# Optimization experiments

Hardware: AMD Instinct MI355X
Metric: run time of the kernel (lower is better)

The kernel has to match this reference:

```python
import jax, jax.numpy as jnp
import numpy as np

D_MODEL = 2048
NUM_HEADS = 16
D_K = D_MODEL // NUM_HEADS
THETA = 10000.0
MAX_SEQ_LEN = 2048
B, S = 2, 2048


def setup_inputs() -> dict:
    key = jax.random.key(0)
    ks = jax.random.split(key, 5)
    x = jax.random.normal(ks[0], (B, S, D_MODEL), dtype=jnp.float32)
    token_positions = jnp.tile(jnp.arange(S, dtype=jnp.int64 if jax.config.jax_enable_x64 else jnp.int32), (B, 1))
    wq = jax.random.normal(ks[1], (D_MODEL, D_MODEL), dtype=jnp.float32)
    wk = jax.random.normal(ks[2], (D_MODEL, D_MODEL), dtype=jnp.float32)
    wv = jax.random.normal(ks[3], (D_MODEL, D_MODEL), dtype=jnp.float32)
    wo = jax.random.normal(ks[4], (D_MODEL, D_MODEL), dtype=jnp.float32)
    return {"x": x, "token_positions": token_positions, "wq": wq, "wk": wk, "wv": wv, "wo": wo}


def _rope_tables():
    # inv freqs: exp(arange(0,d_k,2) * (-log(theta)/d_k))  -> [d_k/2]
    inv_freq = jnp.exp(jnp.arange(0, D_K, 2, dtype=jnp.float32) * (-np.log(THETA) / D_K))
    m = jnp.arange(MAX_SEQ_LEN, dtype=jnp.float32)[:, None]  # [L,1]
    ang = m * inv_freq[None, :]                               # [L, d_k/2]
    return jnp.cos(ang), jnp.sin(ang)


def _apply_rope(x, token_positions, cos_tab, sin_tab):
    # x: [B, H, S, d_k]; token_positions: [B, S]
    cos = cos_tab[token_positions][:, None, :, :]  # [B,1,S,d_k/2]
    sin = sin_tab[token_positions][:, None, :, :]
    xe = x[..., 0::2]
    xo = x[..., 1::2]
    re = xe * cos - xo * sin
    ro = xo * cos + xe * sin
    out = jnp.stack([re, ro], axis=-1).reshape(x.shape)
    return out


def reference(x, token_positions, wq, wk, wv, wo):
    b, s, _ = x.shape
    cos_tab, sin_tab = _rope_tables()

    def split_heads(t):  # [B,S,D] -> [B,H,S,d_k]
        return t.reshape(b, s, NUM_HEADS, D_K).transpose(0, 2, 1, 3)

    q = _apply_rope(split_heads(x @ wq), token_positions, cos_tab, sin_tab)
    k = _apply_rope(split_heads(x @ wk), token_positions, cos_tab, sin_tab)
    v = split_heads(x @ wv)

    scores = jnp.einsum("bhqd,bhkd->bhqk", q, k) / jnp.sqrt(jnp.float32(D_K))
    causal = jnp.tril(jnp.ones((s, s), dtype=bool))
    scores = jnp.where(causal[None, None], scores, jnp.float32(-1e9))
    attn = jax.nn.softmax(scores, axis=-1)
    out = jnp.einsum("bhqk,bhkd->bhqd", attn, v)
    out = out.transpose(0, 2, 1, 3).reshape(b, s, D_MODEL)
    return out @ wo
```

## Files before the change

kernel.cpp:

```cpp
#include <hip/hip_runtime.h>
#include <hip/hip_bf16.h>
#include <cstdio>

namespace {

constexpr int kSeq = 2048;
constexpr int kDModel = 2048;
constexpr int kHeads = 16;
constexpr int kDk = 128;
constexpr int kBatch = 2;
constexpr int kM = kBatch * kSeq;
constexpr float kQScale = 0.08838834764831845f;

typedef __bf16 bf16_t;
typedef __bf16 bf16x8 __attribute__((ext_vector_type(8)));
typedef __bf16 bf16x4 __attribute__((ext_vector_type(4)));
typedef float f32x4 __attribute__((ext_vector_type(4)));
typedef short s16x4 __attribute__((ext_vector_type(4)));

__device__ __forceinline__ f32x4 mfma32(bf16x8 a, bf16x8 b, f32x4 c) {
  return __builtin_amdgcn_mfma_f32_16x16x32_bf16(a, b, c, 0, 0, 0);
}

#if __has_builtin(__builtin_amdgcn_mfma_f32_16x16x16_bf16)
__device__ __forceinline__ f32x4 mfma16(bf16x4 a, bf16x4 b, f32x4 c) {
  return __builtin_amdgcn_mfma_f32_16x16x16_bf16(a, b, c, 0, 0, 0);
}
#else
__device__ __forceinline__ f32x4 mfma16(bf16x4 a, bf16x4 b, f32x4 c) {
  union U { bf16x4 b; s16x4 s; } ua, ub;
  ua.b = a; ub.b = b;
  return __builtin_amdgcn_mfma_f32_16x16x16bf16_1k(ua.s, ub.s, c, 0, 0, 0);
}
#endif

using gas_void = const __attribute__((address_space(1))) void;
using las_void = __attribute__((address_space(3))) void;

__device__ __forceinline__ void gload_lds16(const bf16_t* g, bf16_t* l) {
  __builtin_amdgcn_global_load_lds((gas_void*)g, (las_void*)l, 16, 0, 0);
}

__global__ void k_rope_table(float* __restrict__ cost, float* __restrict__ sint) {
  const int p = blockIdx.x;
  const int i = threadIdx.x;
  const double inv = exp(-(double)(2 * i) * 9.210340371976184 / 128.0);
  const double ang = (double)p * inv;
  cost[p * 64 + i] = (float)cos(ang);
  sint[p * 64 + i] = (float)sin(ang);
}

__global__ void k_split_x(const float* __restrict__ x, bf16_t* __restrict__ xh,
                          bf16_t* __restrict__ xl, int n) {
  const int idx = (blockIdx.x * blockDim.x + threadIdx.x) * 4;
  if (idx >= n) return;
  const float4 v = *(const float4*)(x + idx);
  const float vv[4] = {v.x, v.y, v.z, v.w};
  bf16x4 hv, lv;
#pragma unroll
  for (int j = 0; j < 4; ++j) {
    const bf16_t h = (bf16_t)vv[j];
    hv[j] = h;
    lv[j] = (bf16_t)(vv[j] - (float)h);
  }
  *(bf16x4*)(xh + idx) = hv;
  *(bf16x4*)(xl + idx) = lv;
}

__global__ void k_transpose_w(const float* __restrict__ w, bf16_t* __restrict__ wth,
                              bf16_t* __restrict__ wtl) {
  __shared__ float tile[32][33];
  const int bx = blockIdx.x * 32;
  const int by = blockIdx.y * 32;
  const int tx = threadIdx.x, ty = threadIdx.y;
#pragma unroll
  for (int i = 0; i < 32; i += 8)
    tile[ty + i][tx] = w[(size_t)(by + ty + i) * kDModel + bx + tx];
  __syncthreads();
#pragma unroll
  for (int i = 0; i < 32; i += 8) {
    const float v = tile[tx][ty + i];
    const size_t o = (size_t)(bx + ty + i) * kDModel + by + tx;
    const bf16_t h = (bf16_t)v;
    wth[o] = h;
    if (wtl) wtl[o] = (bf16_t)(v - (float)h);
  }
}

template <int TERMS, int EPI>
__global__ __launch_bounds__(256) void k_gemm(
    const bf16_t* __restrict__ Ah, const bf16_t* __restrict__ Al,
    const bf16_t* __restrict__ Bh, const bf16_t* __restrict__ Bl,
    void* __restrict__ O0, void* __restrict__ O1,
    const int* __restrict__ tokpos, const float* __restrict__ cost,
    const float* __restrict__ sint, float scale, int M, int N, int K) {
  __shared__ __align__(16) bf16_t sAh[128 * 32];
  __shared__ __align__(16) bf16_t sBh[128 * 32];
  __shared__ __align__(16) bf16_t sAl[TERMS == 3 ? 128 * 32 : 8];
  __shared__ __align__(16) bf16_t sBl[TERMS == 3 ? 128 * 32 : 8];

  const int tid = threadIdx.x;
  const int wid = tid >> 6;
  const int lane = tid & 63;
  const int lo = lane & 15, hi = lane >> 4;
  const int wr = wid >> 1, wc = wid & 1;
  const int flat = blockIdx.x + blockIdx.y * gridDim.x;
  const int wgid = (flat & 7) * ((gridDim.x * gridDim.y) >> 3) + (flat >> 3);
  const int m0 = (wgid / gridDim.x) * 128, n0 = (wgid % gridDim.x) * 128;

  f32x4 acc[4][4];
  const f32x4 z = {0.f, 0.f, 0.f, 0.f};
#pragma unroll
  for (int i = 0; i < 4; ++i)
#pragma unroll
    for (int j = 0; j < 4; ++j) acc[i][j] = z;

  const int rr = wid * 16 + (lane >> 2);
  const int kk = (lane & 3) * 8;

  for (int k0 = 0; k0 < K; k0 += 32) {
    __syncthreads();
    {
      const bf16_t* gA = Ah + (size_t)(m0 + rr) * K + k0 + kk;
      gload_lds16(gA, sAh + wid * 512);
      gload_lds16(gA + (size_t)64 * K, sAh + 2048 + wid * 512);
      const bf16_t* gB = Bh + (size_t)(n0 + rr) * K + k0 + kk;
      gload_lds16(gB, sBh + wid * 512);
      gload_lds16(gB + (size_t)64 * K, sBh + 2048 + wid * 512);
      if constexpr (TERMS == 3) {
        const bf16_t* gAl = Al + (size_t)(m0 + rr) * K + k0 + kk;
        gload_lds16(gAl, sAl + wid * 512);
        gload_lds16(gAl + (size_t)64 * K, sAl + 2048 + wid * 512);
        const bf16_t* gBl = Bl + (size_t)(n0 + rr) * K + k0 + kk;
        gload_lds16(gBl, sBl + wid * 512);
        gload_lds16(gBl + (size_t)64 * K, sBl + 2048 + wid * 512);
      }
    }
    __syncthreads();
    bf16x8 fah[4], fbh[4];
#pragma unroll
    for (int mi = 0; mi < 4; ++mi)
      fah[mi] = *(const bf16x8*)(sAh + (wr * 64 + mi * 16 + lo) * 32 + 8 * hi);
#pragma unroll
    for (int ni = 0; ni < 4; ++ni)
      fbh[ni] = *(const bf16x8*)(sBh + (wc * 64 + ni * 16 + lo) * 32 + 8 * hi);
    if constexpr (TERMS == 3) {
      bf16x8 fal[4], fbl[4];
#pragma unroll
      for (int mi = 0; mi < 4; ++mi)
        fal[mi] = *(const bf16x8*)(sAl + (wr * 64 + mi * 16 + lo) * 32 + 8 * hi);
#pragma unroll
      for (int ni = 0; ni < 4; ++ni)
        fbl[ni] = *(const bf16x8*)(sBl + (wc * 64 + ni * 16 + lo) * 32 + 8 * hi);
#pragma unroll
      for (int mi = 0; mi < 4; ++mi)
#pragma unroll
        for (int ni = 0; ni < 4; ++ni) {
          acc[mi][ni] = mfma32(fah[mi], fbh[ni], acc[mi][ni]);
          acc[mi][ni] = mfma32(fah[mi], fbl[ni], acc[mi][ni]);
          acc[mi][ni] = mfma32(fal[mi], fbh[ni], acc[mi][ni]);
        }
    } else {
#pragma unroll
      for (int mi = 0; mi < 4; ++mi)
#pragma unroll
        for (int ni = 0; ni < 4; ++ni)
          acc[mi][ni] = mfma32(fah[mi], fbh[ni], acc[mi][ni]);
    }
  }

  if constexpr (EPI == 0) {
    float* C = (float*)O0;
#pragma unroll
    for (int mi = 0; mi < 4; ++mi)
#pragma unroll
      for (int ni = 0; ni < 4; ++ni)
#pragma unroll
        for (int r = 0; r < 4; ++r) {
          const int row = m0 + wr * 64 + mi * 16 + hi * 4 + r;
          const int col = n0 + wc * 64 + ni * 16 + lo;
          C[(size_t)row * N + col] = acc[mi][ni][r];
        }
  } else if constexpr (EPI == 1) {
    bf16_t* Xh = (bf16_t*)O0;
    bf16_t* Xl = (bf16_t*)O1;
    const int is64 = (tokpos[1] == 0) ? 1 : 0;
#pragma unroll
    for (int mi = 0; mi < 4; ++mi) {
#pragma unroll
      for (int r = 0; r < 4; ++r) {
        const int row = m0 + wr * 64 + mi * 16 + hi * 4 + r;
        const int pos = is64 ? tokpos[2 * row] : tokpos[row];
#pragma unroll
        for (int ni = 0; ni < 4; ++ni) {
          const int col = n0 + wc * 64 + ni * 16 + lo;
          const float v = acc[mi][ni][r] * scale;
          const float pv = __shfl_xor(v, 1);
          const int ip = (col & 127) >> 1;
          const float c = cost[pos * 64 + ip];
          const float sn = sint[pos * 64 + ip];
          const float sgn = (lo & 1) ? sn : -sn;
          const float rv = v * c + pv * sgn;
          const bf16_t hb = (bf16_t)rv;
          const size_t o = (size_t)row * N + col;
          Xh[o] = hb;
          Xl[o] = (bf16_t)(rv - (float)hb);
        }
      }
    }
  } else {
    bf16_t* VT = (bf16_t*)O0;
#pragma unroll
    for (int mi = 0; mi < 4; ++mi)
#pragma unroll
      for (int ni = 0; ni < 4; ++ni) {
        const int col = n0 + wc * 64 + ni * 16 + lo;
        const int h = col >> 7, d = col & 127;
        const int rowb = m0 + wr * 64 + mi * 16 + hi * 4;
        const int b = rowb >> 11, s = rowb & (kSeq - 1);
        bf16x4 ov;
#pragma unroll
        for (int r = 0; r < 4; ++r) ov[r] = (bf16_t)acc[mi][ni][r];
        *(bf16x4*)(VT + ((size_t)((b * kHeads + h) * kDk + d)) * kSeq + s) = ov;
      }
  }
}

__global__ __launch_bounds__(256) void k_attn3(
    const bf16_t* __restrict__ Qh, const bf16_t* __restrict__ Ql,
    const bf16_t* __restrict__ Kh, const bf16_t* __restrict__ Kl,
    const bf16_t* __restrict__ VT, bf16_t* __restrict__ Ob) {
  __shared__ __align__(16) bf16_t sK[2][2][32 * 128];
  __shared__ __align__(16) bf16_t sV[2][128 * 32];

  const int tid = threadIdx.x;
  const int wid = tid >> 6, lane = tid & 63;
  const int lo = lane & 15, hi = lane >> 4;
  const int flat = blockIdx.x + blockIdx.y * gridDim.x;
  const int j = flat >> 3;
  const int bh = (flat & 7) * 4 + (j & 3);
  const int qi = 15 - (j >> 2);
  const int b = bh >> 4, h = bh & 15;
  const int q0 = qi * 128;
  const int qw = q0 + wid * 32;

  bf16x8 qhf[4][2], qlf[4][2];
  {
    const size_t qbase =
        (size_t)(b * kSeq + qw + lo) * kDModel + h * kDk + hi * 8;
#pragma unroll
    for (int qt = 0; qt < 2; ++qt)
#pragma unroll
      for (int ks = 0; ks < 4; ++ks) {
        const size_t o = qbase + (size_t)qt * 16 * kDModel + ks * 32;
        qhf[ks][qt] = *(const bf16x8*)(Qh + o);
        qlf[ks][qt] = *(const bf16x8*)(Ql + o);
      }
  }

  const int rK = wid * 8 + (lane >> 4);
  const int gK0 = ((lane & 15) ^ (rK & 7)) * 8;
  const bf16_t* pKh0 = Kh + (size_t)(b * kSeq + rK) * kDModel + h * kDk + gK0;
  const bf16_t* pKh1 = pKh0 + (size_t)4 * kDModel + ((gK0 ^ 32) - gK0);
  const bf16_t* pKl0 = Kl + (pKh0 - Kh);
  const bf16_t* pKl1 = Kl + (pKh1 - Kh);
  const int dV = wid * 32 + (lane >> 2);
  const int gV = ((lane & 3) ^ ((dV >> 1) & 3)) * 8;
  const bf16_t* pV0 = VT + (size_t)(bh * kDk + dV) * kSeq + gV;
  const bf16_t* pV1 = pV0 + (size_t)16 * kSeq;
  const int ldsK = (wid * 8) * 128;
  const int ldsV = (wid * 32) * 32;

  f32x4 of[8][2];
  const f32x4 z = {0.f, 0.f, 0.f, 0.f};
#pragma unroll
  for (int di = 0; di < 8; ++di) {
    of[di][0] = z;
    of[di][1] = z;
  }
  float m[2] = {-3e38f, -3e38f};
  float l[2] = {0.f, 0.f};

  const int nkv = 4 * qi + 4;

  auto STAGE = [&](int buf, int t) {
    const size_t ko = (size_t)t * 32 * kDModel;
    const size_t vo = (size_t)t * 32;
    bf16_t* dk = sK[buf][0] + ldsK;
    bf16_t* dl = sK[buf][1] + ldsK;
    gload_lds16(pKh0 + ko, dk);
    gload_lds16(pKh1 + ko, dk + 512);
    gload_lds16(pKl0 + ko, dl);
    gload_lds16(pKl1 + ko, dl + 512);
    bf16_t* dv = sV[buf] + ldsV;
    gload_lds16(pV0 + vo, dv);
    gload_lds16(pV1 + vo, dv + 512);
  };

  STAGE(0, 0);
  __syncthreads();

  for (int t = 0; t < nkv; ++t) {
    const int kv0 = t * 32;
    if (t + 1 < nkv) STAGE((t + 1) & 1, t + 1);

    if (kv0 <= qw + 31) {
      const bf16_t* bKh = sK[t & 1][0];
      const bf16_t* bKl = sK[t & 1][1];
      const bf16_t* bV = sV[t & 1];
      const bool maskedw = (kv0 + 31 > qw);

      f32x4 st[2][2];
      st[0][0] = z; st[0][1] = z; st[1][0] = z; st[1][1] = z;
#pragma unroll
      for (int kt = 0; kt < 2; ++kt) {
#pragma unroll
        for (int ks = 0; ks < 4; ++ks) {
          const int krow = kt * 16 + lo;
          const int ka = krow * 128 + (((ks * 4 + hi) ^ (krow & 7)) * 8);
          const bf16x8 kh8 = *(const bf16x8*)(bKh + ka);
          const bf16x8 kl8 = *(const bf16x8*)(bKl + ka);
#pragma unroll
          for (int qt = 0; qt < 2; ++qt) {
            st[kt][qt] = mfma32(kh8, qhf[ks][qt], st[kt][qt]);
            st[kt][qt] = mfma32(kh8, qlf[ks][qt], st[kt][qt]);
            st[kt][qt] = mfma32(kl8, qhf[ks][qt], st[kt][qt]);
          }
        }
      }

      bf16x4 pb[2][2];
#pragma unroll
      for (int qt = 0; qt < 2; ++qt) {
        const int q = qw + qt * 16 + lo;
        float mt = -3e38f;
#pragma unroll
        for (int kt = 0; kt < 2; ++kt)
#pragma unroll
          for (int r = 0; r < 4; ++r) {
            float s = st[kt][qt][r];
            if (maskedw && (kv0 + kt * 16 + hi * 4 + r > q)) s = -1e30f;
            st[kt][qt][r] = s;
            mt = fmaxf(mt, s);
          }
        mt = fmaxf(mt, __shfl_xor(mt, 16));
        mt = fmaxf(mt, __shfl_xor(mt, 32));
        const float mnew = fmaxf(m[qt], mt);
        const float corr = __expf(m[qt] - mnew);
        float rs = 0.f;
#pragma unroll
        for (int kt = 0; kt < 2; ++kt) {
          bf16x4 pv;
#pragma unroll
          for (int r = 0; r < 4; ++r) {
            const float pp = __expf(st[kt][qt][r] - mnew);
            rs += pp;
            pv[r] = (bf16_t)pp;
          }
          pb[kt][qt] = pv;
        }
        rs += __shfl_xor(rs, 16);
        rs += __shfl_xor(rs, 32);
        l[qt] = l[qt] * corr + rs;
        m[qt] = mnew;
#pragma unroll
        for (int di = 0; di < 8; ++di) of[di][qt] = of[di][qt] * corr;
      }

#pragma unroll
      for (int di = 0; di < 8; ++di) {
        const int d = di * 16 + lo;
#pragma unroll
        for (int kt = 0; kt < 2; ++kt) {
          const int c = (kt * 2 + (hi >> 1)) ^ ((d >> 1) & 3);
          const bf16x4 vf = *(const bf16x4*)(bV + d * 32 + c * 8 + (hi & 1) * 4);
          of[di][0] = mfma16(vf, pb[kt][0], of[di][0]);
          of[di][1] = mfma16(vf, pb[kt][1], of[di][1]);
        }
      }
    }
    __syncthreads();
  }

#pragma unroll
  for (int qt = 0; qt < 2; ++qt) {
    const float linv = 1.f / l[qt];
    const size_t ob =
        (size_t)(b * kSeq + qw + qt * 16 + lo) * kDModel + h * kDk + hi * 4;
#pragma unroll
    for (int di = 0; di < 8; ++di) {
      bf16x4 ov;
#pragma unroll
      for (int r = 0; r < 4; ++r) ov[r] = (bf16_t)(of[di][qt][r] * linv);
      *(bf16x4*)(Ob + ob + di * 16) = ov;
    }
  }
}

}

extern "C" void kernel_launch(void* const* d_in, const int* in_sizes, int n_in,
                              void* d_out, int out_size, void* d_ws, size_t ws_size,
                              hipStream_t stream) {
  (void)in_sizes; (void)n_in; (void)out_size;
  const float* x = (const float*)d_in[0];
  const int* tokpos = (const int*)d_in[1];
  const float* wq = (const float*)d_in[2];
  const float* wk = (const float*)d_in[3];
  const float* wv = (const float*)d_in[4];
  const float* wo = (const float*)d_in[5];
  float* out = (float*)d_out;

  char* p = (char*)d_ws;
  auto take = [&](size_t bytes) { char* q = p; p += bytes; return q; };
  float* cost = (float*)take((size_t)kSeq * 64 * sizeof(float));
  float* sint = (float*)take((size_t)kSeq * 64 * sizeof(float));
  const size_t mat = (size_t)kM * kDModel * sizeof(bf16_t);
  const size_t wmat = (size_t)kDModel * kDModel * sizeof(bf16_t);
  bf16_t* xh = (bf16_t*)take(mat);
  bf16_t* xl = (bf16_t*)take(mat);
  bf16_t* wqth = (bf16_t*)take(wmat);
  bf16_t* wqtl = (bf16_t*)take(wmat);
  bf16_t* wkth = (bf16_t*)take(wmat);
  bf16_t* wktl = (bf16_t*)take(wmat);
  bf16_t* wvt = (bf16_t*)take(wmat);
  bf16_t* wot = (bf16_t*)take(wmat);
  bf16_t* qh = (bf16_t*)take(mat);
  bf16_t* ql = (bf16_t*)take(mat);
  bf16_t* kh = (bf16_t*)take(mat);
  bf16_t* kl = (bf16_t*)take(mat);
  bf16_t* vt = (bf16_t*)take(mat);
  bf16_t* ob = (bf16_t*)take(mat);
  if ((size_t)(p - (char*)d_ws) > ws_size) {
    fprintf(stderr, "MHA: workspace too small: need %zu have %zu\n",
            (size_t)(p - (char*)d_ws), ws_size);
    return;
  }

  k_rope_table<<<dim3(kSeq), dim3(64), 0, stream>>>(cost, sint);
  k_split_x<<<dim3((kM * kDModel) / (256 * 4)), dim3(256), 0, stream>>>(
      x, xh, xl, kM * kDModel);
  {
    dim3 tb(32, 8), tg(kDModel / 32, kDModel / 32);
    k_transpose_w<<<tg, tb, 0, stream>>>(wq, wqth, wqtl);
    k_transpose_w<<<tg, tb, 0, stream>>>(wk, wkth, wktl);
    k_transpose_w<<<tg, tb, 0, stream>>>(wv, wvt, nullptr);
    k_transpose_w<<<tg, tb, 0, stream>>>(wo, wot, nullptr);
  }
  const dim3 gg(kDModel / 128, kM / 128);
  k_gemm<3, 1><<<gg, 256, 0, stream>>>(xh, xl, wqth, wqtl, qh, ql, tokpos, cost,
                                       sint, kQScale, kM, kDModel, kDModel);
  k_gemm<3, 1><<<gg, 256, 0, stream>>>(xh, xl, wkth, wktl, kh, kl, tokpos, cost,
                                       sint, 1.0f, kM, kDModel, kDModel);
  k_gemm<1, 2><<<gg, 256, 0, stream>>>(xh, nullptr, wvt, nullptr, vt, nullptr,
                                       nullptr, nullptr, nullptr, 1.0f, kM,
                                       kDModel, kDModel);
  k_attn3<<<dim3(kSeq / 128, kBatch * kHeads), dim3(256), 0, stream>>>(
      qh, ql, kh, kl, vt, ob);
  k_gemm<1, 0><<<gg, 256, 0, stream>>>(ob, nullptr, wot, nullptr, out, nullptr,
                                       nullptr, nullptr, nullptr, 1.0f, kM,
                                       kDModel, kDModel);
}
```

Measured before the change: 511.5 us.

## Pair causal query tiles per block with 64-wide KV tiles and lazy rescale

The attention kernel now runs 512 threads per block. Each block pairs a long causal query tile (15-p) with a short one (p), so its 8 waves share one K/V stream and the causal workload is balanced across blocks. KV tiles grow from 32 to 64 rows, with new LDS swizzles, which halves the loop trips and barriers per query tile. The online-softmax rescale is skipped unless some row's max grows by more than 8, which trades a little exp headroom for fewer multiplies on the output accumulators. LDS usage doubles and register pressure rises with the launch-bounds change.

```diff
diff --git a/kernel.cpp b/kernel.cpp
--- a/kernel.cpp
+++ b/kernel.cpp
@@ -226,23 +226,24 @@
   }
 }
 
-__global__ __launch_bounds__(256) void k_attn3(
+__global__ __launch_bounds__(512, 2) void k_attn4(
     const bf16_t* __restrict__ Qh, const bf16_t* __restrict__ Ql,
     const bf16_t* __restrict__ Kh, const bf16_t* __restrict__ Kl,
     const bf16_t* __restrict__ VT, bf16_t* __restrict__ Ob) {
-  __shared__ __align__(16) bf16_t sK[2][2][32 * 128];
-  __shared__ __align__(16) bf16_t sV[2][128 * 32];
+  __shared__ __align__(16) bf16_t sK[2][2][64 * 128];
+  __shared__ __align__(16) bf16_t sV[2][128 * 64];
 
   const int tid = threadIdx.x;
   const int wid = tid >> 6, lane = tid & 63;
   const int lo = lane & 15, hi = lane >> 4;
-  const int flat = blockIdx.x + blockIdx.y * gridDim.x;
+  const int flat = blockIdx.x;
   const int j = flat >> 3;
   const int bh = (flat & 7) * 4 + (j & 3);
-  const int qi = 15 - (j >> 2);
+  const int p = j >> 2;
   const int b = bh >> 4, h = bh & 15;
-  const int q0 = qi * 128;
-  const int qw = q0 + wid * 32;
+  const int qiW = (wid < 4) ? (15 - p) : p;
+  const int qw = qiW * 128 + (wid & 3) * 32;
+  const int nkv = 2 * (15 - p) + 2;
 
   bf16x8 qhf[4][2], qlf[4][2];
   {
@@ -258,18 +259,20 @@
       }
   }
 
-  const int rK = wid * 8 + (lane >> 4);
-  const int gK0 = ((lane & 15) ^ (rK & 7)) * 8;
-  const bf16_t* pKh0 = Kh + (size_t)(b * kSeq + rK) * kDModel + h * kDk + gK0;
-  const bf16_t* pKh1 = pKh0 + (size_t)4 * kDModel + ((gK0 ^ 32) - gK0);
+  const int rK0 = wid * 8 + (lane >> 4);
+  const int gK0 = ((lane & 15) ^ (rK0 & 15)) * 8;
+  const int gK1 = ((lane & 15) ^ ((rK0 + 4) & 15)) * 8;
+  const bf16_t* pKh0 = Kh + (size_t)(b * kSeq + rK0) * kDModel + h * kDk + gK0;
+  const bf16_t* pKh1 = Kh + (size_t)(b * kSeq + rK0 + 4) * kDModel + h * kDk + gK1;
   const bf16_t* pKl0 = Kl + (pKh0 - Kh);
   const bf16_t* pKl1 = Kl + (pKh1 - Kh);
-  const int dV = wid * 32 + (lane >> 2);
-  const int gV = ((lane & 3) ^ ((dV >> 1) & 3)) * 8;
-  const bf16_t* pV0 = VT + (size_t)(bh * kDk + dV) * kSeq + gV;
-  const bf16_t* pV1 = pV0 + (size_t)16 * kSeq;
+  const int dV0 = wid * 16 + (lane >> 3);
+  const int gV0 = ((lane & 7) ^ (dV0 & 7)) * 8;
+  const int gV1 = ((lane & 7) ^ ((dV0 + 8) & 7)) * 8;
+  const bf16_t* pV0 = VT + (size_t)(bh * kDk + dV0) * kSeq + gV0;
+  const bf16_t* pV1 = VT + (size_t)(bh * kDk + dV0 + 8) * kSeq + gV1;
   const int ldsK = (wid * 8) * 128;
-  const int ldsV = (wid * 32) * 32;
+  const int ldsV = (wid * 16) * 64;
 
   f32x4 of[8][2];
   const f32x4 z = {0.f, 0.f, 0.f, 0.f};
@@ -281,11 +284,9 @@
   float m[2] = {-3e38f, -3e38f};
   float l[2] = {0.f, 0.f};
 
-  const int nkv = 4 * qi + 4;
-
   auto STAGE = [&](int buf, int t) {
-    const size_t ko = (size_t)t * 32 * kDModel;
-    const size_t vo = (size_t)t * 32;
+    const size_t ko = (size_t)t * 64 * kDModel;
+    const size_t vo = (size_t)t * 64;
     bf16_t* dk = sK[buf][0] + ldsK;
     bf16_t* dl = sK[buf][1] + ldsK;
     gload_lds16(pKh0 + ko, dk);
@@ -301,23 +302,27 @@
   __syncthreads();
 
   for (int t = 0; t < nkv; ++t) {
-    const int kv0 = t * 32;
+    const int kv0 = t * 64;
     if (t + 1 < nkv) STAGE((t + 1) & 1, t + 1);
 
     if (kv0 <= qw + 31) {
       const bf16_t* bKh = sK[t & 1][0];
       const bf16_t* bKl = sK[t & 1][1];
       const bf16_t* bV = sV[t & 1];
-      const bool maskedw = (kv0 + 31 > qw);
-
-      f32x4 st[2][2];
-      st[0][0] = z; st[0][1] = z; st[1][0] = z; st[1][1] = z;
-#pragma unroll
-      for (int kt = 0; kt < 2; ++kt) {
+      const bool maskedw = (kv0 + 63 > qw);
+
+      f32x4 st[4][2];
+#pragma unroll
+      for (int kt = 0; kt < 4; ++kt) {
+        st[kt][0] = z;
+        st[kt][1] = z;
+      }
+#pragma unroll
+      for (int kt = 0; kt < 4; ++kt) {
 #pragma unroll
         for (int ks = 0; ks < 4; ++ks) {
           const int krow = kt * 16 + lo;
-          const int ka = krow * 128 + (((ks * 4 + hi) ^ (krow & 7)) * 8);
+          const int ka = krow * 128 + (((ks * 4 + hi) ^ (krow & 15)) * 8);
           const bf16x8 kh8 = *(const bf16x8*)(bKh + ka);
           const bf16x8 kl8 = *(const bf16x8*)(bKl + ka);
 #pragma unroll
@@ -329,13 +334,13 @@
         }
       }
 
-      bf16x4 pb[2][2];
+      bf16x4 pb[4][2];
 #pragma unroll
       for (int qt = 0; qt < 2; ++qt) {
         const int q = qw + qt * 16 + lo;
         float mt = -3e38f;
 #pragma unroll
-        for (int kt = 0; kt < 2; ++kt)
+        for (int kt = 0; kt < 4; ++kt)
 #pragma unroll
           for (int r = 0; r < 4; ++r) {
             float s = st[kt][qt][r];
@@ -345,15 +350,21 @@
           }
         mt = fmaxf(mt, __shfl_xor(mt, 16));
         mt = fmaxf(mt, __shfl_xor(mt, 32));
-        const float mnew = fmaxf(m[qt], mt);
-        const float corr = __expf(m[qt] - mnew);
+        if (!__all(mt <= m[qt] + 8.f)) {
+          const float mnew = fmaxf(m[qt], mt);
+          const float corr = __expf(m[qt] - mnew);
+          l[qt] *= corr;
+#pragma unroll
+          for (int di = 0; di < 8; ++di) of[di][qt] = of[di][qt] * corr;
+          m[qt] = mnew;
+        }
         float rs = 0.f;
 #pragma unroll
-        for (int kt = 0; kt < 2; ++kt) {
+        for (int kt = 0; kt < 4; ++kt) {
           bf16x4 pv;
 #pragma unroll
           for (int r = 0; r < 4; ++r) {
-            const float pp = __expf(st[kt][qt][r] - mnew);
+            const float pp = __expf(st[kt][qt][r] - m[qt]);
             rs += pp;
             pv[r] = (bf16_t)pp;
           }
@@ -361,19 +372,17 @@
         }
         rs += __shfl_xor(rs, 16);
         rs += __shfl_xor(rs, 32);
-        l[qt] = l[qt] * corr + rs;
-        m[qt] = mnew;
-#pragma unroll
-        for (int di = 0; di < 8; ++di) of[di][qt] = of[di][qt] * corr;
+        l[qt] += rs;
       }
 
 #pragma unroll
       for (int di = 0; di < 8; ++di) {
         const int d = di * 16 + lo;
 #pragma unroll
-        for (int kt = 0; kt < 2; ++kt) {
-          const int c = (kt * 2 + (hi >> 1)) ^ ((d >> 1) & 3);
-          const bf16x4 vf = *(const bf16x4*)(bV + d * 32 + c * 8 + (hi & 1) * 4);
+        for (int kt = 0; kt < 4; ++kt) {
+          const int va =
+              d * 64 + (((kt * 2 + (hi >> 1)) ^ (d & 7)) * 8) + (hi & 1) * 4;
+          const bf16x4 vf = *(const bf16x4*)(bV + va);
           of[di][0] = mfma16(vf, pb[kt][0], of[di][0]);
           of[di][1] = mfma16(vf, pb[kt][1], of[di][1]);
         }
@@ -455,8 +464,7 @@
   k_gemm<1, 2><<<gg, 256, 0, stream>>>(xh, nullptr, wvt, nullptr, vt, nullptr,
                                        nullptr, nullptr, nullptr, 1.0f, kM,
                                        kDModel, kDModel);
-  k_attn3<<<dim3(kSeq / 128, kBatch * kHeads), dim3(256), 0, stream>>>(
-      qh, ql, kh, kl, vt, ob);
+  k_attn4<<<dim3(256), dim3(512), 0, stream>>>(qh, ql, kh, kl, vt, ob);
   k_gemm<1, 0><<<gg, 256, 0, stream>>>(ob, nullptr, wot, nullptr, out, nullptr,
                                        nullptr, nullptr, nullptr, 1.0f, kM,
                                        kDModel, kDModel);
```

Result: faster. 467.4 us (-8.6%).
